# Kernel optimization log

Measured on AMD Instinct MI355X. Metric: run time of the kernel, lower is better.

## Reference

```python
import jax, jax.numpy as jnp
import numpy as np

N = 100000
E = 1600000
H = 128
IN = 16
OUT = 16
L = 3
G = 256  # number of graphs
EPS = 1e-12


def setup_inputs() -> dict:
    key = jax.random.key(0)
    ks = jax.random.split(key, 24)
    s = 0.05
    inp = {
        "x": jax.random.normal(ks[0], (N, IN), jnp.float32),
        "pos": jax.random.normal(ks[1], (N, 3), jnp.float32),
        "edge_index": jax.random.randint(ks[2], (2, E), 0, N, jnp.int64),
        "batch": jnp.sort(jax.random.randint(ks[3], (N,), 0, G, jnp.int64)),
        # node_lin: Linear(IN,H), ReLU, Linear(H,H)
        "node_W1": jax.random.normal(ks[4], (IN, H), jnp.float32) * s,
        "node_b1": jnp.zeros((H,), jnp.float32),
        "node_W2": jax.random.normal(ks[5], (H, H), jnp.float32) * s,
        "node_b2": jnp.zeros((H,), jnp.float32),
        # per-layer local_nn: Linear(H+4,H), ReLU, Linear(H,H)  (stacked over L)
        "local_W1": jax.random.normal(ks[6], (L, H + 4, H), jnp.float32) * s,
        "local_b1": jnp.zeros((L, H), jnp.float32),
        "local_W2": jax.random.normal(ks[7], (L, H, H), jnp.float32) * s,
        "local_b2": jnp.zeros((L, H), jnp.float32),
        # per-layer global_nn: Linear(H,H), ReLU, Linear(H,H)
        "global_W1": jax.random.normal(ks[8], (L, H, H), jnp.float32) * s,
        "global_b1": jnp.zeros((L, H), jnp.float32),
        "global_W2": jax.random.normal(ks[9], (L, H, H), jnp.float32) * s,
        "global_b2": jnp.zeros((L, H), jnp.float32),
        # heads
        "lin1_W": jax.random.normal(ks[10], (H, H // 2), jnp.float32) * s,
        "lin1_b": jnp.zeros((H // 2,), jnp.float32),
        "lin2_W": jax.random.normal(ks[11], (H // 2, OUT), jnp.float32) * s,
        "lin2_b": jnp.zeros((OUT,), jnp.float32),
    }
    return inp


def _angle(v1, v2):
    c = jnp.cross(v1, v2, axis=1)
    return jnp.arctan2(jnp.linalg.norm(c, axis=1), jnp.sum(v1 * v2, axis=1))


def reference(x, pos, edge_index, batch,
              node_W1, node_b1, node_W2, node_b2,
              local_W1, local_b1, local_W2, local_b2,
              global_W1, global_b1, global_W2, global_b2,
              lin1_W, lin1_b, lin2_W, lin2_b):
    src = edge_index[0]  # j (source)
    dst = edge_index[1]  # i (target, aggregation index)

    normal = pos / (jnp.linalg.norm(pos, axis=-1, keepdims=True) + EPS)

    pos_i, pos_j = pos[dst], pos[src]
    n_i, n_j = normal[dst], normal[src]
    pseudo = pos_j - pos_i  # [E, 3]
    # point-pair features [E, 4] (constant across layers since pos is fixed)
    ppf = jnp.stack([
        jnp.linalg.norm(pseudo, axis=1),
        _angle(n_i, pseudo),
        _angle(n_j, pseudo),
        _angle(n_i, n_j),
    ], axis=1)

    # node_lin (x is 2D -> MLP path; embedding path unused)
    h = jax.nn.relu(x @ node_W1 + node_b1) @ node_W2 + node_b2  # [N, H]

    for l in range(L):
        msg = jnp.concatenate([h[src], ppf], axis=1)  # [E, H+4]
        msg = jax.nn.relu(msg @ local_W1[l] + local_b1[l]) @ local_W2[l] + local_b2[l]
        agg = jax.ops.segment_sum(msg, dst, num_segments=N)  # scatter-add to nodes
        h = jax.nn.relu(agg @ global_W1[l] + global_b1[l]) @ global_W2[l] + global_b2[l]
        h = jax.nn.relu(h)

    out = jax.nn.relu(h @ lin1_W + lin1_b) @ lin2_W + lin2_b  # [N, OUT]
    return jax.ops.segment_sum(out, batch, num_segments=G)  # [G, OUT]
```

## Files before the change

kernel.cpp:

```cpp
#include <hip/hip_runtime.h>

#define NN 100000
#define NE 1600000
#define HD 128
#define NL 3
#define NG 256
#define NB 196
#define BCAP 56

typedef __attribute__((ext_vector_type(8))) short short8;
typedef __attribute__((ext_vector_type(4))) float floatx4;
typedef __attribute__((ext_vector_type(2))) _Float16 half2v;

static __device__ __forceinline__ unsigned short f2bf(float f) {
    unsigned int u = __float_as_uint(f);
    u += 0x7fffu + ((u >> 16) & 1u);
    return (unsigned short)(u >> 16);
}
static __device__ __forceinline__ float bf2f(unsigned short h) {
    return __uint_as_float(((unsigned int)h) << 16);
}
static __device__ __forceinline__ float angle3(float ax, float ay, float az,
                                               float bx, float by, float bz) {
    float cx = ay*bz - az*by;
    float cy = az*bx - ax*bz;
    float cz = ax*by - ay*bx;
    float cn = sqrtf(cx*cx + cy*cy + cz*cz);
    float d  = ax*bx + ay*by + az*bz;
    return atan2f(cn, d);
}

union U32H2 { unsigned int u; half2v h; };
static __device__ __forceinline__ half2v u2h(unsigned int x) { U32H2 t; t.u = x; return t.h; }
static __device__ __forceinline__ unsigned int h2u(half2v x) { U32H2 t; t.h = x; return t.u; }


struct PrepSrcs { const float* p[14]; };

__global__ void k_prep(PrepSrcs s, unsigned short* __restrict__ dst) {
    int mat = blockIdx.y;
    int N = (mat == 13) ? 64 : 128;
    int e = blockIdx.x * 256 + threadIdx.x;
    if (e >= N * 128) return;
    int n = e >> 7, k = e & 127;
    dst[mat * 16384 + n * 128 + k] = f2bf(s.p[mat][k * N + n]);
}


__global__ void k_pn(const float* __restrict__ pos, float4* __restrict__ pn, int n) {
    int i = blockIdx.x * blockDim.x + threadIdx.x;
    if (i >= n) return;
    float x = pos[3*i], y = pos[3*i+1], z = pos[3*i+2];
    float inv = 1.0f / (sqrtf(x*x + y*y + z*z) + 1e-12f);
    pn[2*i]   = make_float4(x, y, z, 0.0f);
    pn[2*i+1] = make_float4(x*inv, y*inv, z*inv, 0.0f);
}


__global__ __launch_bounds__(256) void k_bcount(const int* __restrict__ ei,
                                                int* __restrict__ bcnt, int e) {
    __shared__ int cnt[NB];
    int tid = threadIdx.x;
    for (int i = tid; i < NB; i += 256) cnt[i] = 0;
    __syncthreads();
    int i0 = blockIdx.x * 4096 + tid * 16;
    if (i0 < e) {
#pragma unroll
        for (int q = 0; q < 4; q++) {
            int4 d4 = *(const int4*)(ei + NE + i0 + q * 4);
            atomicAdd(&cnt[d4.x >> 9], 1);
            atomicAdd(&cnt[d4.y >> 9], 1);
            atomicAdd(&cnt[d4.z >> 9], 1);
            atomicAdd(&cnt[d4.w >> 9], 1);
        }
    }
    __syncthreads();
    for (int i = tid; i < NB; i += 256)
        if (cnt[i]) atomicAdd(&bcnt[i], cnt[i]);
}

__global__ void k_bscan(const int* __restrict__ bcnt, int* __restrict__ bbase,
                        int* __restrict__ bcursor, int* __restrict__ starts) {
    if (threadIdx.x == 0 && blockIdx.x == 0) {
        int acc = 0;
        for (int b = 0; b < NB; b++) {
            bbase[b] = acc; bcursor[b] = acc;
            acc += bcnt[b];
        }
        bbase[NB] = acc;
        starts[NN] = NE;
    }
}

__global__ __launch_bounds__(256) void k_bscatter(const int* __restrict__ ei,
                                                  int* __restrict__ bcursor,
                                                  unsigned int* __restrict__ bids, int e) {
    __shared__ int lcnt[NB];
    __shared__ unsigned int lbuf[NB * BCAP];
    int tid = threadIdx.x;
    for (int i = tid; i < NB; i += 256) lcnt[i] = 0;
    __syncthreads();
    int i0 = blockIdx.x * 4096 + tid * 16;
    if (i0 < e) {
#pragma unroll
        for (int q = 0; q < 4; q++) {
            int4 d4 = *(const int4*)(ei + NE + i0 + q * 4);
            int ds[4] = {d4.x, d4.y, d4.z, d4.w};
#pragma unroll
            for (int r = 0; r < 4; r++) {
                int d = ds[r];
                int b = d >> 9;
                unsigned int w = ((unsigned int)(d & 511) << 23) | (unsigned int)(i0 + q * 4 + r);
                int pos = atomicAdd(&lcnt[b], 1);
                if (pos < BCAP) lbuf[b * BCAP + pos] = w;
                else { int p = atomicAdd(&bcursor[b], 1); bids[p] = w; }
            }
        }
    }
    __syncthreads();
    if (tid < NB) {
        int c = lcnt[tid];
        if (c > BCAP) c = BCAP;
        if (c > 0) {
            int base = atomicAdd(&bcursor[tid], c);
            for (int k = 0; k < c; k++) bids[base + k] = lbuf[tid * BCAP + k];
        }
    }
}

__global__ __launch_bounds__(256) void k_bfinal(const unsigned int* __restrict__ bids,
                                                const int* __restrict__ bbase,
                                                int* __restrict__ perm,
                                                int* __restrict__ starts,
                                                int* __restrict__ deg) {
    __shared__ int s1[512];
    __shared__ int s2[256];
    int tid = threadIdx.x;
    int b = blockIdx.x;
    int node0 = b << 9;
    int base0 = bbase[b];
    int cnt = bbase[b + 1] - base0;
    s1[2 * tid] = 0; s1[2 * tid + 1] = 0;
    __syncthreads();
    for (int j = tid; j < cnt; j += 256)
        atomicAdd(&s1[bids[base0 + j] >> 23], 1);
    __syncthreads();
    int a0 = s1[2 * tid], a1 = s1[2 * tid + 1];
    s2[tid] = a0 + a1;
    __syncthreads();
    for (int off = 1; off < 256; off <<= 1) {
        int v = (tid >= off) ? s2[tid - off] : 0;
        __syncthreads();
        s2[tid] += v;
        __syncthreads();
    }
    int pairBase = (tid ? s2[tid - 1] : 0);
    int e0 = base0 + pairBase;
    int e1 = e0 + a0;
    int n0 = node0 + 2 * tid;
    if (n0 < NN)     { starts[n0] = e0;     deg[n0] = a0; }
    if (n0 + 1 < NN) { starts[n0 + 1] = e1; deg[n0 + 1] = a1; }
    s1[2 * tid] = e0; s1[2 * tid + 1] = e1;
    __syncthreads();
    for (int j = tid; j < cnt; j += 256) {
        unsigned int w = bids[base0 + j];
        int loc = w >> 23;
        int id = (int)(w & 0x7fffffu);
        int p = atomicAdd(&s1[loc], 1);
        perm[p] = id;
    }
}

__global__ void k_ppf_sorted(const int* __restrict__ perm, const int* __restrict__ ei,
                             const float4* __restrict__ pn,
                             int* __restrict__ ssrc, uint2* __restrict__ sppf, int e) {
    int j = blockIdx.x * blockDim.x + threadIdx.x;
    if (j >= e) return;
    int i = perm[j];
    int s = ei[i];
    int d = ei[NE + i];
    float4 ps_ = pn[2*s], ns_ = pn[2*s+1];
    float4 pd_ = pn[2*d], nd_ = pn[2*d+1];
    float px = ps_.x - pd_.x;
    float py = ps_.y - pd_.y;
    float pz = ps_.z - pd_.z;
    float f0 = sqrtf(px*px + py*py + pz*pz);
    float f1 = angle3(nd_.x, nd_.y, nd_.z, px, py, pz);
    float f2 = angle3(ns_.x, ns_.y, ns_.z, px, py, pz);
    float f3 = angle3(nd_.x, nd_.y, nd_.z, ns_.x, ns_.y, ns_.z);
    ssrc[j] = s;
    half2v h01 = { (_Float16)f0, (_Float16)f1 };
    half2v h23 = { (_Float16)f2, (_Float16)f3 };
    uint2 w;
    w.x = h2u(h01);
    w.y = h2u(h23);
    sppf[j] = w;
}


__global__ void k_node_lin1(const float* __restrict__ x, const float* __restrict__ W1,
                            const float* __restrict__ b1, unsigned short* __restrict__ u, int n) {
    __shared__ float sW[16 * HD];
    __shared__ float sb[HD];
    __shared__ float sx[16 * 16];
    int tid = threadIdx.x;
    for (int idx = tid; idx < 16 * HD; idx += 256) sW[idx] = W1[idx];
    if (tid < HD) sb[tid] = b1[tid];
    int r0 = blockIdx.x * 16;
    for (int idx = tid; idx < 16 * 16; idx += 256) {
        int r = r0 + (idx >> 4);
        sx[idx] = (r < n) ? x[r * 16 + (idx & 15)] : 0.0f;
    }
    __syncthreads();
    int col = tid & 127;
    int rsub = tid >> 7;
    float wcol[16];
#pragma unroll
    for (int k = 0; k < 16; k++) wcol[k] = sW[k * HD + col];
    float bb = sb[col];
    for (int rr = rsub; rr < 16; rr += 2) {
        int r = r0 + rr;
        if (r >= n) break;
        float acc = bb;
#pragma unroll
        for (int k = 0; k < 16; k++) acc = fmaf(sx[rr * 16 + k], wcol[k], acc);
        u[r * HD + col] = f2bf(fmaxf(acc, 0.0f));
    }
}


template <int NC, int EPI>
__global__ __launch_bounds__(256, 2) void k_gemm128(
    const unsigned short* __restrict__ A, const unsigned short* __restrict__ Wt,
    const float* __restrict__ bias, const int* __restrict__ deg,
    const float* __restrict__ b2, unsigned short* __restrict__ out, int n) {
    constexpr int SK = 136;
    __shared__ unsigned short Bt[NC * SK];
    int tid = threadIdx.x;
    for (int idx = tid; idx < NC * 16; idx += 256) {
        int c = idx >> 4, k8 = idx & 15;
        *(short8*)&Bt[c * SK + k8 * 8] = ((const short8*)Wt)[idx];
    }
    __syncthreads();

    int wave = tid >> 6, lane = tid & 63;
    int quad = lane >> 4, m = lane & 15;
    int rowBase = blockIdx.x * 128 + wave * 32;

    short8 a[2][4];
#pragma unroll
    for (int rt = 0; rt < 2; rt++) {
        int r = rowBase + rt * 16 + m;
        int rc = (r < n) ? r : (n - 1);
        const unsigned short* ap = A + (size_t)rc * 128 + quad * 8;
#pragma unroll
        for (int s = 0; s < 4; s++) a[rt][s] = *(const short8*)(ap + s * 32);
    }

    constexpr int NT = NC / 16;
    floatx4 acc[2][NT];
    floatx4 z = {0.0f, 0.0f, 0.0f, 0.0f};
#pragma unroll
    for (int rt = 0; rt < 2; rt++)
#pragma unroll
        for (int ct = 0; ct < NT; ct++) acc[rt][ct] = z;

#pragma unroll
    for (int ct = 0; ct < NT; ct++) {
        const unsigned short* bp = &Bt[(ct * 16 + m) * SK + quad * 8];
#pragma unroll
        for (int s = 0; s < 4; s++) {
            short8 b = *(const short8*)(bp + s * 32);
            acc[0][ct] = __builtin_amdgcn_mfma_f32_16x16x32_bf16(a[0][s], b, acc[0][ct], 0, 0, 0);
            acc[1][ct] = __builtin_amdgcn_mfma_f32_16x16x32_bf16(a[1][s], b, acc[1][ct], 0, 0, 0);
        }
    }

    float dv[2][4];
    if (EPI == 2) {
#pragma unroll
        for (int rt = 0; rt < 2; rt++)
#pragma unroll
            for (int r = 0; r < 4; r++) {
                int orow = rowBase + rt * 16 + quad * 4 + r;
                dv[rt][r] = (orow < n) ? (float)deg[orow] : 0.0f;
            }
    }

#pragma unroll
    for (int ct = 0; ct < NT; ct++) {
        int col = ct * 16 + m;
        float bv = (EPI == 0) ? 0.0f : ((EPI == 2) ? b2[col] : bias[col]);
#pragma unroll
        for (int rt = 0; rt < 2; rt++) {
#pragma unroll
            for (int r = 0; r < 4; r++) {
                int orow = rowBase + rt * 16 + quad * 4 + r;
                if (orow < n) {
                    float v = acc[rt][ct][r];
                    if (EPI == 1 || EPI == 3) v += bv;
                    if (EPI == 2) v += dv[rt][r] * bv;
                    if (EPI == 3) v = fmaxf(v, 0.0f);
                    out[(size_t)orow * NC + col] = f2bf(v);
                }
            }
        }
    }
}


#define SKW 136
#define SKT 136

__global__ __launch_bounds__(256) void k_gchain(
    const unsigned short* __restrict__ S, const unsigned short* __restrict__ W2t,
    const unsigned short* __restrict__ GW1t, const unsigned short* __restrict__ GW2t,
    const int* __restrict__ deg, const float* __restrict__ b2,
    const float* __restrict__ Gb1, const float* __restrict__ Gb2,
    unsigned short* __restrict__ out, int n) {
    __shared__ unsigned short LW[128 * SKW];
    __shared__ unsigned short LT[64 * SKT];
    __shared__ float sb2[128], sg1[128], sg2[128];
    int tid = threadIdx.x;
    if (tid < 128) { sb2[tid] = b2[tid]; sg1[tid] = Gb1[tid]; sg2[tid] = Gb2[tid]; }
    for (int idx = tid; idx < 128 * 16; idx += 256) {
        int c = idx >> 4, k8 = idx & 15;
        *(short8*)&LW[c * SKW + k8 * 8] = ((const short8*)W2t)[idx];
    }
    int wave = tid >> 6, lane = tid & 63, quad = lane >> 4, m = lane & 15;
    int rowA = blockIdx.x * 64 + wave * 16 + m;
    int rcA = rowA < n ? rowA : n - 1;
    short8 a[4];
    {
        const unsigned short* ap = S + (size_t)rcA * 128 + quad * 8;
#pragma unroll
        for (int s = 0; s < 4; s++) a[s] = *(const short8*)(ap + s * 32);
    }
    __syncthreads();

    floatx4 acc[8];
    floatx4 z = {0.0f, 0.0f, 0.0f, 0.0f};
#pragma unroll
    for (int ct = 0; ct < 8; ct++) acc[ct] = z;
#pragma unroll
    for (int ct = 0; ct < 8; ct++) {
        const unsigned short* bp = &LW[(ct * 16 + m) * SKW + quad * 8];
#pragma unroll
        for (int s = 0; s < 4; s++) {
            short8 b = *(const short8*)(bp + s * 32);
            acc[ct] = __builtin_amdgcn_mfma_f32_16x16x32_bf16(a[s], b, acc[ct], 0, 0, 0);
        }
    }
    int rowC = wave * 16 + quad * 4;
    float dv[4];
#pragma unroll
    for (int r = 0; r < 4; r++) {
        int gr = blockIdx.x * 64 + rowC + r;
        dv[r] = (float)deg[gr < n ? gr : n - 1];
    }
#pragma unroll
    for (int ct = 0; ct < 8; ct++) {
        int col = ct * 16 + m;
        float bb = sb2[col];
#pragma unroll
        for (int r = 0; r < 4; r++)
            LT[(rowC + r) * SKT + col] = f2bf(acc[ct][r] + dv[r] * bb);
    }
    __syncthreads();

    for (int idx = tid; idx < 128 * 16; idx += 256) {
        int c = idx >> 4, k8 = idx & 15;
        *(short8*)&LW[c * SKW + k8 * 8] = ((const short8*)GW1t)[idx];
    }
    {
        const unsigned short* tp = &LT[(wave * 16 + m) * SKT + quad * 8];
#pragma unroll
        for (int s = 0; s < 4; s++) a[s] = *(const short8*)(tp + s * 32);
    }
    __syncthreads();

#pragma unroll
    for (int ct = 0; ct < 8; ct++) acc[ct] = z;
#pragma unroll
    for (int ct = 0; ct < 8; ct++) {
        const unsigned short* bp = &LW[(ct * 16 + m) * SKW + quad * 8];
#pragma unroll
        for (int s = 0; s < 4; s++) {
            short8 b = *(const short8*)(bp + s * 32);
            acc[ct] = __builtin_amdgcn_mfma_f32_16x16x32_bf16(a[s], b, acc[ct], 0, 0, 0);
        }
    }
#pragma unroll
    for (int ct = 0; ct < 8; ct++) {
        int col = ct * 16 + m;
        float bb = sg1[col];
#pragma unroll
        for (int r = 0; r < 4; r++)
            LT[(rowC + r) * SKT + col] = f2bf(fmaxf(acc[ct][r] + bb, 0.0f));
    }
    __syncthreads();

    for (int idx = tid; idx < 128 * 16; idx += 256) {
        int c = idx >> 4, k8 = idx & 15;
        *(short8*)&LW[c * SKW + k8 * 8] = ((const short8*)GW2t)[idx];
    }
    {
        const unsigned short* tp = &LT[(wave * 16 + m) * SKT + quad * 8];
#pragma unroll
        for (int s = 0; s < 4; s++) a[s] = *(const short8*)(tp + s * 32);
    }
    __syncthreads();

#pragma unroll
    for (int ct = 0; ct < 8; ct++) acc[ct] = z;
#pragma unroll
    for (int ct = 0; ct < 8; ct++) {
        const unsigned short* bp = &LW[(ct * 16 + m) * SKW + quad * 8];
#pragma unroll
        for (int s = 0; s < 4; s++) {
            short8 b = *(const short8*)(bp + s * 32);
            acc[ct] = __builtin_amdgcn_mfma_f32_16x16x32_bf16(a[s], b, acc[ct], 0, 0, 0);
        }
    }
#pragma unroll
    for (int ct = 0; ct < 8; ct++) {
        int col = ct * 16 + m;
        float bb = sg2[col];
#pragma unroll
        for (int r = 0; r < 4; r++) {
            int gr = blockIdx.x * 64 + rowC + r;
            if (gr < n) out[(size_t)gr * 128 + col] = f2bf(fmaxf(acc[ct][r] + bb, 0.0f));
        }
    }
}


#if __has_builtin(__builtin_amdgcn_fdot2)
#define HAVE_FDOT2 1
#else
#define HAVE_FDOT2 0
#endif

static __device__ __forceinline__ void agg_edge(unsigned int u, uint2 q,
                                                half2v wA0, half2v wB0, half2v wA1, half2v wB1,
                                                float2 bb, float& a0, float& a1) {
    float tlo = __uint_as_float(u << 16);
    float thi = __uint_as_float(u & 0xffff0000u);
#if HAVE_FDOT2
    half2v p01 = u2h(q.x), p23 = u2h(q.y);
    float g0 = __builtin_amdgcn_fdot2(p01, wA0,
               __builtin_amdgcn_fdot2(p23, wB0, bb.x + tlo, false), false);
    float g1 = __builtin_amdgcn_fdot2(p01, wA1,
               __builtin_amdgcn_fdot2(p23, wB1, bb.y + thi, false), false);
#else
    half2v p01 = u2h(q.x), p23 = u2h(q.y);
    float px = (float)p01.x, py = (float)p01.y, pz = (float)p23.x, pw = (float)p23.y;
    float g0 = fmaf(px, (float)wA0.x, fmaf(py, (float)wA0.y,
               fmaf(pz, (float)wB0.x, fmaf(pw, (float)wB0.y, bb.x + tlo))));
    float g1 = fmaf(px, (float)wA1.x, fmaf(py, (float)wA1.y,
               fmaf(pz, (float)wB1.x, fmaf(pw, (float)wB1.y, bb.y + thi))));
#endif
    a0 += fmaxf(g0, 0.0f);
    a1 += fmaxf(g1, 0.0f);
}

__global__ __launch_bounds__(256, 8) void k_agg(
    const int* __restrict__ starts, const int* __restrict__ ssrc,
    const uint2* __restrict__ sppf, const unsigned int* __restrict__ t,
    const float* __restrict__ W1p, const float* __restrict__ b1,
    unsigned int* __restrict__ S, int n) {
    int node = (blockIdx.x * 256 + threadIdx.x) >> 6;
    if (node >= n) return;
    int lane = threadIdx.x & 63;
    int c2 = lane * 2;
    float2 w0 = *(const float2*)(W1p + c2);
    float2 w1 = *(const float2*)(W1p + 128 + c2);
    float2 w2 = *(const float2*)(W1p + 256 + c2);
    float2 w3 = *(const float2*)(W1p + 384 + c2);
    float2 bb = *(const float2*)(b1 + c2);
    half2v wA0 = { (_Float16)w0.x, (_Float16)w1.x };
    half2v wB0 = { (_Float16)w2.x, (_Float16)w3.x };
    half2v wA1 = { (_Float16)w0.y, (_Float16)w1.y };
    half2v wB1 = { (_Float16)w2.y, (_Float16)w3.y };
    int e0 = __builtin_amdgcn_readfirstlane(starts[node]);
    int e1 = __builtin_amdgcn_readfirstlane(starts[node + 1]);
    float a0 = 0.0f, a1 = 0.0f;
    int e = e0;
    for (; e + 4 <= e1; e += 4) {
        int s0 = ssrc[e], s1 = ssrc[e + 1], s2 = ssrc[e + 2], s3 = ssrc[e + 3];
        uint2 q0 = sppf[e], q1 = sppf[e + 1], q2 = sppf[e + 2], q3 = sppf[e + 3];
        unsigned int u0 = t[(size_t)s0 * 64 + lane];
        unsigned int u1 = t[(size_t)s1 * 64 + lane];
        unsigned int u2 = t[(size_t)s2 * 64 + lane];
        unsigned int u3 = t[(size_t)s3 * 64 + lane];
        agg_edge(u0, q0, wA0, wB0, wA1, wB1, bb, a0, a1);
        agg_edge(u1, q1, wA0, wB0, wA1, wB1, bb, a0, a1);
        agg_edge(u2, q2, wA0, wB0, wA1, wB1, bb, a0, a1);
        agg_edge(u3, q3, wA0, wB0, wA1, wB1, bb, a0, a1);
    }
    for (; e < e1; e++) {
        int s0 = ssrc[e];
        uint2 q0 = sppf[e];
        unsigned int u0 = t[(size_t)s0 * 64 + lane];
        agg_edge(u0, q0, wA0, wB0, wA1, wB1, bb, a0, a1);
    }
    unsigned int r = ((unsigned int)f2bf(a1) << 16) | f2bf(a0);
    S[(size_t)node * 64 + lane] = r;
}


__global__ void k_head2(const unsigned short* __restrict__ v, const float* __restrict__ W,
                        const float* __restrict__ b, const int* __restrict__ batch,
                        float* __restrict__ outg, int n) {
    __shared__ float sW[64 * 16];
    __shared__ float sb[16];
    __shared__ float sacc[64][17];
    __shared__ int sbid[64];
    int tid = threadIdx.x;
    for (int idx = tid; idx < 64 * 16; idx += 256) sW[idx] = W[idx];
    if (tid < 16) sb[tid] = b[tid];
    int r0 = blockIdx.x * 64;
    if (tid < 64) {
        int r = r0 + tid;
        sbid[tid] = (r < n) ? batch[r] : -1;
    }
    __syncthreads();
    int rl = tid >> 4, c = tid & 15;
#pragma unroll
    for (int i = 0; i < 4; i++) {
        int row = rl + i * 16;
        int r = r0 + row;
        float acc = 0.0f;
        if (r < n) {
            const unsigned int* vr = (const unsigned int*)(v + (size_t)r * 64);
            acc = sb[c];
#pragma unroll
            for (int k2 = 0; k2 < 32; k2++) {
                unsigned int u = vr[k2];
                acc = fmaf(__uint_as_float(u << 16), sW[(2 * k2) * 16 + c], acc);
                acc = fmaf(__uint_as_float(u & 0xffff0000u), sW[(2 * k2 + 1) * 16 + c], acc);
            }
        }
        sacc[row][c] = acc;
    }
    __syncthreads();
    if (tid < 16) {
        int cc = tid;
        float run = 0.0f;
        int cur = sbid[0];
        for (int row = 0; row < 64; row++) {
            int bid = sbid[row];
            if (bid != cur) {
                if (cur >= 0) atomicAdd(&outg[cur * 16 + cc], run);
                run = 0.0f;
                cur = bid;
            }
            run += sacc[row][cc];
        }
        if (cur >= 0) atomicAdd(&outg[cur * 16 + cc], run);
    }
}


extern "C" void kernel_launch(void* const* d_in, const int* in_sizes, int n_in,
                              void* d_out, int out_size, void* d_ws, size_t ws_size,
                              hipStream_t stream) {
    (void)in_sizes; (void)n_in; (void)out_size; (void)ws_size;
    const float* x    = (const float*)d_in[0];
    const float* pos  = (const float*)d_in[1];
    const int*   ei   = (const int*)d_in[2];
    const int*   batch= (const int*)d_in[3];
    const float* nW1  = (const float*)d_in[4];
    const float* nb1  = (const float*)d_in[5];
    const float* nW2  = (const float*)d_in[6];
    const float* nb2  = (const float*)d_in[7];
    const float* lW1  = (const float*)d_in[8];
    const float* lb1  = (const float*)d_in[9];
    const float* lW2  = (const float*)d_in[10];
    const float* lb2  = (const float*)d_in[11];
    const float* gW1  = (const float*)d_in[12];
    const float* gb1  = (const float*)d_in[13];
    const float* gW2  = (const float*)d_in[14];
    const float* gb2  = (const float*)d_in[15];
    const float* l1W  = (const float*)d_in[16];
    const float* l1b  = (const float*)d_in[17];
    const float* l2W  = (const float*)d_in[18];
    const float* l2b  = (const float*)d_in[19];
    float* outg = (float*)d_out;

    char* ws = (char*)d_ws;
    size_t off = 0;
    auto alloc = [&](size_t bytes) -> void* {
        void* p = ws + off;
        off = (off + bytes + 255) & ~(size_t)255;
        return p;
    };
    unsigned short* P0 = (unsigned short*)alloc((size_t)NN * HD * 2);
    unsigned short* P1 = (unsigned short*)alloc((size_t)NN * HD * 2);
    uint2* sppf  = (uint2*)alloc((size_t)NE * 8);
    int* ssrc    = (int*)alloc((size_t)NE * 4);
    float4* pn   = (float4*)alloc((size_t)NN * 32);
    int* deg     = (int*)alloc((size_t)NN * 4);
    int* starts  = (int*)alloc((size_t)(NN + 2) * 4);
    int* bcnt    = (int*)alloc((size_t)(NB + 2) * 4);
    int* bbase   = (int*)alloc((size_t)(NB + 2) * 4);
    int* bcursor = (int*)alloc((size_t)(NB + 2) * 4);
    unsigned short* pw = (unsigned short*)alloc((size_t)14 * 16384 * 2);
    int* perm          = (int*)P0;
    unsigned int* bids = (unsigned int*)((char*)P0 + ((size_t)NE * 4 + 256));

    PrepSrcs ps;
    ps.p[0] = nW2;
    for (int l = 0; l < 3; l++) {
        ps.p[1 + l] = lW1 + (size_t)l * 132 * 128;
        ps.p[4 + l] = lW2 + (size_t)l * 16384;
        ps.p[7 + l] = gW1 + (size_t)l * 16384;
        ps.p[10 + l] = gW2 + (size_t)l * 16384;
    }
    ps.p[13] = l1W;

    hipMemsetAsync(bcnt, 0, (size_t)(NB + 2) * 4, stream);
    hipMemsetAsync(outg, 0, (size_t)NG * 16 * 4, stream);

    k_prep<<<dim3(64, 14), 256, 0, stream>>>(ps, pw);
    k_pn<<<(NN + 255) / 256, 256, 0, stream>>>(pos, pn, NN);
    const int NTILE = (NE + 4095) / 4096;
    k_bcount<<<NTILE, 256, 0, stream>>>(ei, bcnt, NE);
    k_bscan<<<1, 64, 0, stream>>>(bcnt, bbase, bcursor, starts);
    k_bscatter<<<NTILE, 256, 0, stream>>>(ei, bcursor, bids, NE);
    k_bfinal<<<NB, 256, 0, stream>>>(bids, bbase, perm, starts, deg);
    k_ppf_sorted<<<(NE + 255) / 256, 256, 0, stream>>>(perm, ei, pn, ssrc, sppf, NE);

    k_node_lin1<<<(NN + 15) / 16, 256, 0, stream>>>(x, nW1, nb1, P1, NN);
    const int GB = (NN + 127) / 128;
    k_gemm128<128, 1><<<GB, 256, 0, stream>>>(P1, pw, nb2, nullptr, nullptr, P0, NN);

    unsigned short* hbuf = P0;
    unsigned short* obuf = P1;
    const int AGB = (NN * 64 + 255) / 256;
    const int CGB = (NN + 63) / 64;
    for (int l = 0; l < NL; l++) {
        const float* W1p = lW1 + (size_t)l * 132 * 128 + 128 * 128;
        const float* b1  = lb1 + l * 128;
        const float* b2  = lb2 + l * 128;
        const float* Gb1 = gb1 + l * 128;
        const float* Gb2 = gb2 + l * 128;
        const unsigned short* pwW1h = pw + (size_t)(1 + l) * 16384;
        const unsigned short* pwW2  = pw + (size_t)(4 + l) * 16384;
        const unsigned short* pwGW1 = pw + (size_t)(7 + l) * 16384;
        const unsigned short* pwGW2 = pw + (size_t)(10 + l) * 16384;
        k_gemm128<128, 0><<<GB, 256, 0, stream>>>(hbuf, pwW1h, nullptr, nullptr, nullptr, obuf, NN);
        k_agg<<<AGB, 256, 0, stream>>>(starts, ssrc, sppf, (const unsigned int*)obuf,
                                       W1p, b1, (unsigned int*)hbuf, NN);
        k_gchain<<<CGB, 256, 0, stream>>>(hbuf, pwW2, pwGW1, pwGW2, deg, b2, Gb1, Gb2, obuf, NN);
        unsigned short* tmp = hbuf; hbuf = obuf; obuf = tmp;
    }
    k_gemm128<64, 3><<<GB, 256, 0, stream>>>(hbuf, pw + (size_t)13 * 16384, l1b,
                                             nullptr, nullptr, obuf, NN);
    k_head2<<<(NN + 63) / 64, 256, 0, stream>>>(obuf, l2W, l2b, batch, outg, NN);
}
```

Before: 610.1 us.

## Process 128 rows per gchain block and unroll aggregation gather by eight

The fused global-MLP chain kernel now handles 128 rows per block, two 16-row tiles per wave, so each weight matrix staged in LDS is reused across twice as many rows. Its three stages are folded into one loop, and the kernel gets a launch-bounds hint of two blocks per CU. The edge aggregation kernel unrolls its gather loop to eight edges to keep more loads in flight, and uses 32-bit shift/or indexing instead of size_t multiplies. The cost is more registers and LDS per block, plus an odd per-row deg reload for the second tile, which may lower occupancy.

```diff
diff --git a/kernel.cpp b/kernel.cpp
--- a/kernel.cpp
+++ b/kernel.cpp
@@ -312,125 +312,98 @@
 #define SKW 136
 #define SKT 136
 
-__global__ __launch_bounds__(256) void k_gchain(
+__global__ __launch_bounds__(256, 2) void k_gchain(
     const unsigned short* __restrict__ S, const unsigned short* __restrict__ W2t,
     const unsigned short* __restrict__ GW1t, const unsigned short* __restrict__ GW2t,
     const int* __restrict__ deg, const float* __restrict__ b2,
     const float* __restrict__ Gb1, const float* __restrict__ Gb2,
     unsigned short* __restrict__ out, int n) {
     __shared__ unsigned short LW[128 * SKW];
-    __shared__ unsigned short LT[64 * SKT];
+    __shared__ unsigned short LT[128 * SKT];
     __shared__ float sb2[128], sg1[128], sg2[128];
     int tid = threadIdx.x;
     if (tid < 128) { sb2[tid] = b2[tid]; sg1[tid] = Gb1[tid]; sg2[tid] = Gb2[tid]; }
-    for (int idx = tid; idx < 128 * 16; idx += 256) {
-        int c = idx >> 4, k8 = idx & 15;
-        *(short8*)&LW[c * SKW + k8 * 8] = ((const short8*)W2t)[idx];
-    }
     int wave = tid >> 6, lane = tid & 63, quad = lane >> 4, m = lane & 15;
-    int rowA = blockIdx.x * 64 + wave * 16 + m;
-    int rcA = rowA < n ? rowA : n - 1;
-    short8 a[4];
-    {
-        const unsigned short* ap = S + (size_t)rcA * 128 + quad * 8;
-#pragma unroll
-        for (int s = 0; s < 4; s++) a[s] = *(const short8*)(ap + s * 32);
-    }
-    __syncthreads();
-
-    floatx4 acc[8];
+    int rowBase = wave * 32;
+    int gBase = blockIdx.x * 128;
+    int rowC = rowBase + quad * 4;
+    const unsigned short* Ws[3] = {W2t, GW1t, GW2t};
     floatx4 z = {0.0f, 0.0f, 0.0f, 0.0f};
-#pragma unroll
-    for (int ct = 0; ct < 8; ct++) acc[ct] = z;
-#pragma unroll
-    for (int ct = 0; ct < 8; ct++) {
-        const unsigned short* bp = &LW[(ct * 16 + m) * SKW + quad * 8];
-#pragma unroll
-        for (int s = 0; s < 4; s++) {
-            short8 b = *(const short8*)(bp + s * 32);
-            acc[ct] = __builtin_amdgcn_mfma_f32_16x16x32_bf16(a[s], b, acc[ct], 0, 0, 0);
-        }
-    }
-    int rowC = wave * 16 + quad * 4;
-    float dv[4];
+    short8 a[2][4];
+#pragma unroll
+    for (int rt = 0; rt < 2; rt++) {
+        int r = gBase + rowBase + rt * 16 + m;
+        int rc = r < n ? r : n - 1;
+        const unsigned short* ap = S + (size_t)rc * 128 + quad * 8;
+#pragma unroll
+        for (int s = 0; s < 4; s++) a[rt][s] = *(const short8*)(ap + s * 32);
+    }
+    float dvd[4];
 #pragma unroll
     for (int r = 0; r < 4; r++) {
-        int gr = blockIdx.x * 64 + rowC + r;
-        dv[r] = (float)deg[gr < n ? gr : n - 1];
-    }
-#pragma unroll
-    for (int ct = 0; ct < 8; ct++) {
-        int col = ct * 16 + m;
-        float bb = sb2[col];
-#pragma unroll
-        for (int r = 0; r < 4; r++)
-            LT[(rowC + r) * SKT + col] = f2bf(acc[ct][r] + dv[r] * bb);
-    }
-    __syncthreads();
-
-    for (int idx = tid; idx < 128 * 16; idx += 256) {
-        int c = idx >> 4, k8 = idx & 15;
-        *(short8*)&LW[c * SKW + k8 * 8] = ((const short8*)GW1t)[idx];
-    }
-    {
-        const unsigned short* tp = &LT[(wave * 16 + m) * SKT + quad * 8];
-#pragma unroll
-        for (int s = 0; s < 4; s++) a[s] = *(const short8*)(tp + s * 32);
-    }
-    __syncthreads();
-
-#pragma unroll
-    for (int ct = 0; ct < 8; ct++) acc[ct] = z;
-#pragma unroll
-    for (int ct = 0; ct < 8; ct++) {
-        const unsigned short* bp = &LW[(ct * 16 + m) * SKW + quad * 8];
-#pragma unroll
-        for (int s = 0; s < 4; s++) {
-            short8 b = *(const short8*)(bp + s * 32);
-            acc[ct] = __builtin_amdgcn_mfma_f32_16x16x32_bf16(a[s], b, acc[ct], 0, 0, 0);
-        }
-    }
-#pragma unroll
-    for (int ct = 0; ct < 8; ct++) {
-        int col = ct * 16 + m;
-        float bb = sg1[col];
-#pragma unroll
-        for (int r = 0; r < 4; r++)
-            LT[(rowC + r) * SKT + col] = f2bf(fmaxf(acc[ct][r] + bb, 0.0f));
-    }
-    __syncthreads();
-
-    for (int idx = tid; idx < 128 * 16; idx += 256) {
-        int c = idx >> 4, k8 = idx & 15;
-        *(short8*)&LW[c * SKW + k8 * 8] = ((const short8*)GW2t)[idx];
-    }
-    {
-        const unsigned short* tp = &LT[(wave * 16 + m) * SKT + quad * 8];
-#pragma unroll
-        for (int s = 0; s < 4; s++) a[s] = *(const short8*)(tp + s * 32);
-    }
-    __syncthreads();
-
-#pragma unroll
-    for (int ct = 0; ct < 8; ct++) acc[ct] = z;
-#pragma unroll
-    for (int ct = 0; ct < 8; ct++) {
-        const unsigned short* bp = &LW[(ct * 16 + m) * SKW + quad * 8];
-#pragma unroll
-        for (int s = 0; s < 4; s++) {
-            short8 b = *(const short8*)(bp + s * 32);
-            acc[ct] = __builtin_amdgcn_mfma_f32_16x16x32_bf16(a[s], b, acc[ct], 0, 0, 0);
-        }
-    }
-#pragma unroll
-    for (int ct = 0; ct < 8; ct++) {
-        int col = ct * 16 + m;
-        float bb = sg2[col];
-#pragma unroll
-        for (int r = 0; r < 4; r++) {
-            int gr = blockIdx.x * 64 + rowC + r;
-            if (gr < n) out[(size_t)gr * 128 + col] = f2bf(fmaxf(acc[ct][r] + bb, 0.0f));
-        }
+        int gr = gBase + rowC + r;
+        dvd[r] = (float)deg[gr < n ? gr : n - 1];
+    }
+
+#pragma unroll
+    for (int st = 0; st < 3; st++) {
+        for (int idx = tid; idx < 128 * 16; idx += 256) {
+            int c = idx >> 4, k8 = idx & 15;
+            *(short8*)&LW[c * SKW + k8 * 8] = ((const short8*)Ws[st])[idx];
+        }
+        if (st > 0) {
+#pragma unroll
+            for (int rt = 0; rt < 2; rt++) {
+                const unsigned short* tp = &LT[(rowBase + rt * 16 + m) * SKT + quad * 8];
+#pragma unroll
+                for (int s = 0; s < 4; s++) a[rt][s] = *(const short8*)(tp + s * 32);
+            }
+        }
+        __syncthreads();
+
+        floatx4 acc[2][8];
+#pragma unroll
+        for (int rt = 0; rt < 2; rt++)
+#pragma unroll
+            for (int ct = 0; ct < 8; ct++) acc[rt][ct] = z;
+#pragma unroll
+        for (int ct = 0; ct < 8; ct++) {
+            const unsigned short* bp = &LW[(ct * 16 + m) * SKW + quad * 8];
+#pragma unroll
+            for (int s = 0; s < 4; s++) {
+                short8 b = *(const short8*)(bp + s * 32);
+                acc[0][ct] = __builtin_amdgcn_mfma_f32_16x16x32_bf16(a[0][s], b, acc[0][ct], 0, 0, 0);
+                acc[1][ct] = __builtin_amdgcn_mfma_f32_16x16x32_bf16(a[1][s], b, acc[1][ct], 0, 0, 0);
+            }
+        }
+#pragma unroll
+        for (int ct = 0; ct < 8; ct++) {
+            int col = ct * 16 + m;
+            float bb = (st == 0) ? sb2[col] : (st == 1 ? sg1[col] : sg2[col]);
+#pragma unroll
+            for (int rt = 0; rt < 2; rt++) {
+#pragma unroll
+                for (int r = 0; r < 4; r++) {
+                    float v = acc[rt][ct][r];
+                    if (st == 0) v += dvd[r] * bb;
+                    else v = fmaxf(v + bb, 0.0f);
+                    int row = rowBase + rt * 16 + quad * 4 + r;
+                    if (st == 0) {
+                        if (rt == 1) {
+                            int gr = gBase + row;
+                            v = acc[rt][ct][r] + (float)deg[gr < n ? gr : n - 1] * bb;
+                        }
+                        LT[row * SKT + col] = f2bf(v);
+                    } else if (st == 1) {
+                        LT[row * SKT + col] = f2bf(v);
+                    } else {
+                        int gr = gBase + row;
+                        if (gr < n) out[(size_t)gr * 128 + col] = f2bf(v);
+                    }
+                }
+            }
+        }
+        __syncthreads();
     }
 }
 
@@ -486,22 +459,44 @@
     int e1 = __builtin_amdgcn_readfirstlane(starts[node + 1]);
     float a0 = 0.0f, a1 = 0.0f;
     int e = e0;
-    for (; e + 4 <= e1; e += 4) {
-        int s0 = ssrc[e], s1 = ssrc[e + 1], s2 = ssrc[e + 2], s3 = ssrc[e + 3];
-        uint2 q0 = sppf[e], q1 = sppf[e + 1], q2 = sppf[e + 2], q3 = sppf[e + 3];
-        unsigned int u0 = t[(size_t)s0 * 64 + lane];
-        unsigned int u1 = t[(size_t)s1 * 64 + lane];
-        unsigned int u2 = t[(size_t)s2 * 64 + lane];
-        unsigned int u3 = t[(size_t)s3 * 64 + lane];
+    for (; e + 8 <= e1; e += 8) {
+        int s0 = ssrc[e],     s1 = ssrc[e + 1], s2 = ssrc[e + 2], s3 = ssrc[e + 3];
+        int s4 = ssrc[e + 4], s5 = ssrc[e + 5], s6 = ssrc[e + 6], s7 = ssrc[e + 7];
+        uint2 q0 = sppf[e],     q1 = sppf[e + 1], q2 = sppf[e + 2], q3 = sppf[e + 3];
+        uint2 q4 = sppf[e + 4], q5 = sppf[e + 5], q6 = sppf[e + 6], q7 = sppf[e + 7];
+        unsigned int u0 = t[((unsigned)s0 << 6) | lane];
+        unsigned int u1 = t[((unsigned)s1 << 6) | lane];
+        unsigned int u2 = t[((unsigned)s2 << 6) | lane];
+        unsigned int u3 = t[((unsigned)s3 << 6) | lane];
+        unsigned int u4 = t[((unsigned)s4 << 6) | lane];
+        unsigned int u5 = t[((unsigned)s5 << 6) | lane];
+        unsigned int u6 = t[((unsigned)s6 << 6) | lane];
+        unsigned int u7 = t[((unsigned)s7 << 6) | lane];
         agg_edge(u0, q0, wA0, wB0, wA1, wB1, bb, a0, a1);
         agg_edge(u1, q1, wA0, wB0, wA1, wB1, bb, a0, a1);
         agg_edge(u2, q2, wA0, wB0, wA1, wB1, bb, a0, a1);
         agg_edge(u3, q3, wA0, wB0, wA1, wB1, bb, a0, a1);
+        agg_edge(u4, q4, wA0, wB0, wA1, wB1, bb, a0, a1);
+        agg_edge(u5, q5, wA0, wB0, wA1, wB1, bb, a0, a1);
+        agg_edge(u6, q6, wA0, wB0, wA1, wB1, bb, a0, a1);
+        agg_edge(u7, q7, wA0, wB0, wA1, wB1, bb, a0, a1);
+    }
+    for (; e + 4 <= e1; e += 4) {
+        int s0 = ssrc[e], s1 = ssrc[e + 1], s2 = ssrc[e + 2], s3 = ssrc[e + 3];
+        uint2 q0 = sppf[e], q1 = sppf[e + 1], q2 = sppf[e + 2], q3 = sppf[e + 3];
+        unsigned int u0 = t[((unsigned)s0 << 6) | lane];
+        unsigned int u1 = t[((unsigned)s1 << 6) | lane];
+        unsigned int u2 = t[((unsigned)s2 << 6) | lane];
+        unsigned int u3 = t[((unsigned)s3 << 6) | lane];
+        agg_edge(u0, q0, wA0, wB0, wA1, wB1, bb, a0, a1);
+        agg_edge(u1, q1, wA0, wB0, wA1, wB1, bb, a0, a1);
+        agg_edge(u2, q2, wA0, wB0, wA1, wB1, bb, a0, a1);
+        agg_edge(u3, q3, wA0, wB0, wA1, wB1, bb, a0, a1);
     }
     for (; e < e1; e++) {
         int s0 = ssrc[e];
         uint2 q0 = sppf[e];
-        unsigned int u0 = t[(size_t)s0 * 64 + lane];
+        unsigned int u0 = t[((unsigned)s0 << 6) | lane];
         agg_edge(u0, q0, wA0, wB0, wA1, wB1, bb, a0, a1);
     }
     unsigned int r = ((unsigned int)f2bf(a1) << 16) | f2bf(a0);
@@ -638,7 +633,6 @@
     unsigned short* hbuf = P0;
     unsigned short* obuf = P1;
     const int AGB = (NN * 64 + 255) / 256;
-    const int CGB = (NN + 63) / 64;
     for (int l = 0; l < NL; l++) {
         const float* W1p = lW1 + (size_t)l * 132 * 128 + 128 * 128;
         const float* b1  = lb1 + l * 128;
@@ -652,7 +646,7 @@
         k_gemm128<128, 0><<<GB, 256, 0, stream>>>(hbuf, pwW1h, nullptr, nullptr, nullptr, obuf, NN);
         k_agg<<<AGB, 256, 0, stream>>>(starts, ssrc, sppf, (const unsigned int*)obuf,
                                        W1p, b1, (unsigned int*)hbuf, NN);
-        k_gchain<<<CGB, 256, 0, stream>>>(hbuf, pwW2, pwGW1, pwGW2, deg, b2, Gb1, Gb2, obuf, NN);
+        k_gchain<<<GB, 256, 0, stream>>>(hbuf, pwW2, pwGW1, pwGW2, deg, b2, Gb1, Gb2, obuf, NN);
         unsigned short* tmp = hbuf; hbuf = obuf; obuf = tmp;
     }
     k_gemm128<64, 3><<<GB, 256, 0, stream>>>(hbuf, pw + (size_t)13 * 16384, l1b,
```

Result: faster. 595.9 us (-2.3%).
